# Kernel tuning notes

Measured on AMD Instinct MI355X. Metric: run time of the kernel, lower is better.

Reference implementation:

```python
import jax, jax.numpy as jnp
import numpy as np

N_NODES = 100000
N_EDGES = 1600000
IN_DIM = 7
HID = 64
OUT_DIM = 1
EPS = 1e-5  # BatchNorm1d eps


def setup_inputs() -> dict:
    key = jax.random.key(0)
    ks = jax.random.split(key, 16)
    x = jax.random.normal(ks[0], (N_NODES, IN_DIM), dtype=jnp.float32)
    edge_index = jax.random.randint(ks[1], (2, N_EDGES), 0, N_NODES)

    def lin(k, din, dout):
        # Glorot-ish init for a [din, dout] weight (x @ W convention)
        return jax.random.normal(k, (din, dout), dtype=jnp.float32) / np.float32(np.sqrt(din))

    inp = {"x": x, "edge_index": edge_index}
    dims = [(IN_DIM, HID), (HID, HID), (HID, HID)]
    i = 2
    for l, (din, dout) in enumerate(dims):
        inp[f"Wl{l}"] = lin(ks[i], din, dout); i += 1   # SAGEConv lin_l (applied to aggregated neighbors), carries bias
        inp[f"bl{l}"] = jnp.zeros((dout,), jnp.float32)
        inp[f"Wr{l}"] = lin(ks[i], din, dout); i += 1   # SAGEConv lin_r (root/self weight, no bias)
        inp[f"g{l}"] = jnp.ones((dout,), jnp.float32)   # BN gamma
        inp[f"be{l}"] = jnp.zeros((dout,), jnp.float32) # BN beta
    inp["Wo"] = lin(ks[i], HID, OUT_DIM); i += 1
    inp["bo"] = jnp.zeros((OUT_DIM,), jnp.float32)
    return inp


def _sage_bn_relu(x, src, dst, Wl, bl, Wr, g, be):
    # SAGEConv(aggr='mean'): out = lin_l(mean_{j->i} x_j) + lin_r(x_i)
    n = x.shape[0]
    msg = x[src]                                               # [E, d] gather
    s = jax.ops.segment_sum(msg, dst, num_segments=n)          # [N, d] scatter-add
    cnt = jax.ops.segment_sum(jnp.ones((src.shape[0],), x.dtype), dst, num_segments=n)
    agg = s / jnp.maximum(cnt, 1.0)[:, None]                   # scatter-mean (isolated nodes -> 0)
    h = agg @ Wl + bl + x @ Wr
    # BatchNorm1d (training-mode batch statistics over nodes)
    mu = h.mean(axis=0)
    var = h.var(axis=0)
    h = g * (h - mu) * jax.lax.rsqrt(var + EPS) + be
    return jax.nn.relu(h)


def reference(x, edge_index, Wl0, bl0, Wr0, g0, be0, Wl1, bl1, Wr1, g1, be1, Wl2, bl2, Wr2, g2, be2, Wo, bo):
    src, dst = edge_index[0], edge_index[1]
    h = _sage_bn_relu(x, src, dst, Wl0, bl0, Wr0, g0, be0)
    h = _sage_bn_relu(h, src, dst, Wl1, bl1, Wr1, g1, be1)
    h = _sage_bn_relu(h, src, dst, Wl2, bl2, Wr2, g2, be2)
    return h @ Wo + bo                                         # [N, 1]
```

## Files before the change

kernel.cpp:

```cpp
#include <hip/hip_runtime.h>

#define EPSV 1e-5f
#define REP 8
#define SBCAP 1280
#define CWIN 16640

static __device__ __forceinline__ ushort f2bf(float f) {
    unsigned u = __float_as_uint(f);
    unsigned r = (u + 0x7FFF + ((u >> 16) & 1)) >> 16;
    return (ushort)r;
}


__global__ __launch_bounds__(256) void sb_scatter(
    const int* __restrict__ src, const int* __restrict__ dst,
    int* __restrict__ sbcnt, int* __restrict__ bbuf, int E, int NSB)
{
    __shared__ int hist[512];
    __shared__ int gbase[512];
    int t = threadIdx.x;
    int r = blockIdx.x & (REP - 1);
    for (int i = t; i < NSB; i += 256) hist[i] = 0;
    __syncthreads();

    int base_i = (blockIdx.x * 256 + t) * 8;
    int d[8], s[8], rk[8];
    int m = E - base_i; m = m < 0 ? 0 : (m > 8 ? 8 : m);
    if (m == 8) {
        int4 da = *reinterpret_cast<const int4*>(dst + base_i);
        int4 db = *reinterpret_cast<const int4*>(dst + base_i + 4);
        int4 sa = *reinterpret_cast<const int4*>(src + base_i);
        int4 sb4 = *reinterpret_cast<const int4*>(src + base_i + 4);
        d[0] = da.x; d[1] = da.y; d[2] = da.z; d[3] = da.w;
        d[4] = db.x; d[5] = db.y; d[6] = db.z; d[7] = db.w;
        s[0] = sa.x; s[1] = sa.y; s[2] = sa.z; s[3] = sa.w;
        s[4] = sb4.x; s[5] = sb4.y; s[6] = sb4.z; s[7] = sb4.w;
    } else {
        for (int k = 0; k < m; ++k) { d[k] = dst[base_i + k]; s[k] = src[base_i + k]; }
    }
    for (int k = 0; k < m; ++k)
        rk[k] = atomicAdd(&hist[d[k] >> 9], 1);
    __syncthreads();

    for (int i = t; i < NSB; i += 256) {
        int c = hist[i];
        gbase[i] = c ? atomicAdd(&sbcnt[(r * NSB + i) * 16], c) : 0;
    }
    __syncthreads();

    for (int k = 0; k < m; ++k) {
        int sbk = d[k] >> 9;
        int pos = gbase[sbk] + rk[k];
        if (pos < SBCAP)
            bbuf[(size_t)(r * NSB + sbk) * SBCAP + pos] = ((d[k] & 511) << 17) | s[k];
    }
}

__global__ __launch_bounds__(512) void sb_build(
    const int* __restrict__ sbcnt, const int* __restrict__ bbuf,
    int2* __restrict__ seg, int* __restrict__ col, int n, int NSB)
{
    __shared__ int cnt[512], off[512], cur[512];
    int sb = blockIdx.x;
    int node0 = sb << 9;
    int t = threadIdx.x;
    cnt[t] = 0;
    __syncthreads();

    for (int r = 0; r < REP; ++r) {
        int c = min(sbcnt[(r * NSB + sb) * 16], SBCAP);
        const int* __restrict__ w = bbuf + (size_t)(r * NSB + sb) * SBCAP;
        for (int i = t; i < c; i += 512) atomicAdd(&cnt[w[i] >> 17], 1);
    }
    __syncthreads();

    if (t < 64) {
        int v[8]; int run = 0;
#pragma unroll
        for (int k = 0; k < 8; ++k) {
            v[k] = run;
            run += (cnt[t * 8 + k] + 15) & ~15;
        }
        int pre = run;
        for (int dd = 1; dd < 64; dd <<= 1) {
            int tm = __shfl_up(pre, dd);
            if (t >= dd) pre += tm;
        }
        int lane_excl = pre - run;
#pragma unroll
        for (int k = 0; k < 8; ++k) off[t * 8 + k] = lane_excl + v[k];
    }
    __syncthreads();

    int colbase = sb * CWIN;
    {
        int node = node0 + t;
        if (node < n) seg[node] = make_int2(colbase + off[t], cnt[t]);
        cur[t] = off[t];
    }
    __syncthreads();

    for (int r = 0; r < REP; ++r) {
        int c = min(sbcnt[(r * NSB + sb) * 16], SBCAP);
        const int* __restrict__ w = bbuf + (size_t)(r * NSB + sb) * SBCAP;
        for (int i = t; i < c; i += 512) {
            int e = w[i];
            int p = atomicAdd(&cur[e >> 17], 1);
            col[colbase + p] = e & 0x1FFFF;
        }
    }
    __syncthreads();
    {
        int pend = off[t] + ((cnt[t] + 15) & ~15);
        for (int p = off[t] + cnt[t]; p < pend; ++p) col[colbase + p] = n;
    }
}


__global__ __launch_bounds__(512) void transform7(
    const float* __restrict__ x,
    const float* __restrict__ Wl, const float* __restrict__ bl, const float* __restrict__ Wr,
    ushort* __restrict__ yl, float* __restrict__ h, int n)
{
    __shared__ float swl[7 * 64], swr[7 * 64], sbl[64];
    for (int i = threadIdx.x; i < 7 * 64; i += 512) { swl[i] = Wl[i]; swr[i] = Wr[i]; }
    if (threadIdx.x < 64) sbl[threadIdx.x] = bl[threadIdx.x];
    __syncthreads();

    if (blockIdx.x == 0 && threadIdx.x < 64) yl[(size_t)n * 64 + threadIdx.x] = 0;

    int lane = threadIdx.x & 63;
    int node = blockIdx.x * 8 + (threadIdx.x >> 6);
    if (node >= n) return;

    float xv = (lane < 7) ? x[(size_t)node * 7 + lane] : 0.f;
    float hl = 0.f, hr = sbl[lane];
#pragma unroll
    for (int k = 0; k < 7; ++k) {
        float xk = __shfl(xv, k);
        hl += xk * swl[k * 64 + lane];
        hr += xk * swr[k * 64 + lane];
    }
    yl[(size_t)node * 64 + lane] = f2bf(hl);
    h[(size_t)node * 64 + lane] = hr;
}


__global__ __launch_bounds__(256) void transform64(
    const float* __restrict__ zin, const float* __restrict__ scale, const float* __restrict__ shift,
    const float* __restrict__ Wl, const float* __restrict__ Wr, const float* __restrict__ bl,
    ushort* __restrict__ yl, float* __restrict__ h, int n)
{
    __shared__ float zt[64][68];
    __shared__ float swl[64 * 64];
    __shared__ float swr[64 * 64];
    __shared__ float ssc[64], ssh[64], sbl[64];

    int t = threadIdx.x;
    if (t < 64) { ssc[t] = scale[t]; ssh[t] = shift[t]; sbl[t] = bl[t]; }
    for (int i = t; i < 4096; i += 256) { swl[i] = Wl[i]; swr[i] = Wr[i]; }
    __syncthreads();

    int node0 = blockIdx.x * 64;
    {
        int m = t >> 2, c4 = (t & 3) * 16;
        int gm = node0 + m;
        if (gm < n) {
            const float4* zp = reinterpret_cast<const float4*>(zin + (size_t)gm * 64 + c4);
#pragma unroll
            for (int j = 0; j < 4; ++j) {
                float4 v = zp[j];
                int c = c4 + j * 4;
                v.x = fmaxf(v.x * ssc[c + 0] + ssh[c + 0], 0.f);
                v.y = fmaxf(v.y * ssc[c + 1] + ssh[c + 1], 0.f);
                v.z = fmaxf(v.z * ssc[c + 2] + ssh[c + 2], 0.f);
                v.w = fmaxf(v.w * ssc[c + 3] + ssh[c + 3], 0.f);
                zt[m][c + 0] = v.x; zt[m][c + 1] = v.y; zt[m][c + 2] = v.z; zt[m][c + 3] = v.w;
            }
        } else {
#pragma unroll
            for (int j = 0; j < 16; ++j) zt[m][c4 + j] = 0.f;
        }
    }
    __syncthreads();

    int ng = t >> 4;
    int cg = t & 15;
    int mb = ng * 4;
    const float* sw = (cg < 8) ? swl : swr;
    int c0 = (cg & 7) * 8;

    float acc[4][8];
#pragma unroll
    for (int i = 0; i < 4; ++i)
#pragma unroll
        for (int j = 0; j < 8; ++j) acc[i][j] = 0.f;

#pragma unroll 4
    for (int k = 0; k < 64; ++k) {
        float z0 = zt[mb + 0][k];
        float z1 = zt[mb + 1][k];
        float z2 = zt[mb + 2][k];
        float z3 = zt[mb + 3][k];
        float4 wa = *reinterpret_cast<const float4*>(sw + k * 64 + c0);
        float4 wb = *reinterpret_cast<const float4*>(sw + k * 64 + c0 + 4);
        float w[8] = {wa.x, wa.y, wa.z, wa.w, wb.x, wb.y, wb.z, wb.w};
#pragma unroll
        for (int j = 0; j < 8; ++j) {
            acc[0][j] += z0 * w[j];
            acc[1][j] += z1 * w[j];
            acc[2][j] += z2 * w[j];
            acc[3][j] += z3 * w[j];
        }
    }

#pragma unroll
    for (int i = 0; i < 4; ++i) {
        int gm = node0 + mb + i;
        if (gm >= n) continue;
        if (cg < 8) {
            uint4 pk;
            pk.x = (unsigned)f2bf(acc[i][0]) | ((unsigned)f2bf(acc[i][1]) << 16);
            pk.y = (unsigned)f2bf(acc[i][2]) | ((unsigned)f2bf(acc[i][3]) << 16);
            pk.z = (unsigned)f2bf(acc[i][4]) | ((unsigned)f2bf(acc[i][5]) << 16);
            pk.w = (unsigned)f2bf(acc[i][6]) | ((unsigned)f2bf(acc[i][7]) << 16);
            *reinterpret_cast<uint4*>(yl + (size_t)gm * 64 + c0) = pk;
        } else {
            float* dp = h + (size_t)gm * 64 + c0;
            *reinterpret_cast<float4*>(dp) =
                make_float4(acc[i][0] + sbl[c0 + 0], acc[i][1] + sbl[c0 + 1],
                            acc[i][2] + sbl[c0 + 2], acc[i][3] + sbl[c0 + 3]);
            *reinterpret_cast<float4*>(dp + 4) =
                make_float4(acc[i][4] + sbl[c0 + 4], acc[i][5] + sbl[c0 + 5],
                            acc[i][6] + sbl[c0 + 6], acc[i][7] + sbl[c0 + 7]);
        }
    }
}


__global__ __launch_bounds__(512) void gather_kernel(
    const ushort* __restrict__ yl, float* __restrict__ h,
    const int* __restrict__ col, const int2* __restrict__ seg, int n)
{
    int lane = threadIdx.x & 63;
    int node0 = blockIdx.x * 16 + (threadIdx.x >> 6) * 2;
    if (node0 >= n) return;
    int node1 = node0 + 1;

    int4 sp = *reinterpret_cast<const int4*>(&seg[node0]);
    int s0 = __builtin_amdgcn_readfirstlane(sp.x);
    int d0 = __builtin_amdgcn_readfirstlane(sp.y);
    int s1 = __builtin_amdgcn_readfirstlane(sp.z);
    int d1 = __builtin_amdgcn_readfirstlane(sp.w);
    if (node1 >= n) d1 = 0;
    int pc0 = (d0 + 15) & ~15;
    int pc1 = (d1 + 15) & ~15;
    int pcm = max(pc0, pc1);
    const int* __restrict__ cp0 = col + s0;
    const int* __restrict__ cp1 = col + s1;

    bool hi = lane >= 32;
    unsigned cl = (unsigned)(lane & 31);
    const unsigned* __restrict__ ylu = reinterpret_cast<const unsigned*>(yl);

    float alo0 = 0.f, ahi0 = 0.f, alo1 = 0.f, ahi1 = 0.f;
    for (int j0 = 0; j0 < pcm; j0 += 16) {
        if (j0 < pc0) {
            int4 ia = *reinterpret_cast<const int4*>(cp0 + j0);
            int4 ib = *reinterpret_cast<const int4*>(cp0 + j0 + 4);
            int4 ic = *reinterpret_cast<const int4*>(cp0 + j0 + 8);
            int4 id = *reinterpret_cast<const int4*>(cp0 + j0 + 12);
            unsigned p0 = (unsigned)(hi ? ia.y : ia.x);
            unsigned p1 = (unsigned)(hi ? ia.w : ia.z);
            unsigned p2 = (unsigned)(hi ? ib.y : ib.x);
            unsigned p3 = (unsigned)(hi ? ib.w : ib.z);
            unsigned p4 = (unsigned)(hi ? ic.y : ic.x);
            unsigned p5 = (unsigned)(hi ? ic.w : ic.z);
            unsigned p6 = (unsigned)(hi ? id.y : id.x);
            unsigned p7 = (unsigned)(hi ? id.w : id.z);
            unsigned u0 = ylu[(p0 << 5) + cl];
            unsigned u1 = ylu[(p1 << 5) + cl];
            unsigned u2 = ylu[(p2 << 5) + cl];
            unsigned u3 = ylu[(p3 << 5) + cl];
            unsigned u4 = ylu[(p4 << 5) + cl];
            unsigned u5 = ylu[(p5 << 5) + cl];
            unsigned u6 = ylu[(p6 << 5) + cl];
            unsigned u7 = ylu[(p7 << 5) + cl];
            alo0 += __uint_as_float(u0 << 16);      ahi0 += __uint_as_float(u0 & 0xFFFF0000u);
            alo0 += __uint_as_float(u1 << 16);      ahi0 += __uint_as_float(u1 & 0xFFFF0000u);
            alo0 += __uint_as_float(u2 << 16);      ahi0 += __uint_as_float(u2 & 0xFFFF0000u);
            alo0 += __uint_as_float(u3 << 16);      ahi0 += __uint_as_float(u3 & 0xFFFF0000u);
            alo0 += __uint_as_float(u4 << 16);      ahi0 += __uint_as_float(u4 & 0xFFFF0000u);
            alo0 += __uint_as_float(u5 << 16);      ahi0 += __uint_as_float(u5 & 0xFFFF0000u);
            alo0 += __uint_as_float(u6 << 16);      ahi0 += __uint_as_float(u6 & 0xFFFF0000u);
            alo0 += __uint_as_float(u7 << 16);      ahi0 += __uint_as_float(u7 & 0xFFFF0000u);
        }
        if (j0 < pc1) {
            int4 ia = *reinterpret_cast<const int4*>(cp1 + j0);
            int4 ib = *reinterpret_cast<const int4*>(cp1 + j0 + 4);
            int4 ic = *reinterpret_cast<const int4*>(cp1 + j0 + 8);
            int4 id = *reinterpret_cast<const int4*>(cp1 + j0 + 12);
            unsigned p0 = (unsigned)(hi ? ia.y : ia.x);
            unsigned p1 = (unsigned)(hi ? ia.w : ia.z);
            unsigned p2 = (unsigned)(hi ? ib.y : ib.x);
            unsigned p3 = (unsigned)(hi ? ib.w : ib.z);
            unsigned p4 = (unsigned)(hi ? ic.y : ic.x);
            unsigned p5 = (unsigned)(hi ? ic.w : ic.z);
            unsigned p6 = (unsigned)(hi ? id.y : id.x);
            unsigned p7 = (unsigned)(hi ? id.w : id.z);
            unsigned u0 = ylu[(p0 << 5) + cl];
            unsigned u1 = ylu[(p1 << 5) + cl];
            unsigned u2 = ylu[(p2 << 5) + cl];
            unsigned u3 = ylu[(p3 << 5) + cl];
            unsigned u4 = ylu[(p4 << 5) + cl];
            unsigned u5 = ylu[(p5 << 5) + cl];
            unsigned u6 = ylu[(p6 << 5) + cl];
            unsigned u7 = ylu[(p7 << 5) + cl];
            alo1 += __uint_as_float(u0 << 16);      ahi1 += __uint_as_float(u0 & 0xFFFF0000u);
            alo1 += __uint_as_float(u1 << 16);      ahi1 += __uint_as_float(u1 & 0xFFFF0000u);
            alo1 += __uint_as_float(u2 << 16);      ahi1 += __uint_as_float(u2 & 0xFFFF0000u);
            alo1 += __uint_as_float(u3 << 16);      ahi1 += __uint_as_float(u3 & 0xFFFF0000u);
            alo1 += __uint_as_float(u4 << 16);      ahi1 += __uint_as_float(u4 & 0xFFFF0000u);
            alo1 += __uint_as_float(u5 << 16);      ahi1 += __uint_as_float(u5 & 0xFFFF0000u);
            alo1 += __uint_as_float(u6 << 16);      ahi1 += __uint_as_float(u6 & 0xFFFF0000u);
            alo1 += __uint_as_float(u7 << 16);      ahi1 += __uint_as_float(u7 & 0xFFFF0000u);
        }
    }
    alo0 += __shfl_xor(alo0, 32);
    ahi0 += __shfl_xor(ahi0, 32);
    alo1 += __shfl_xor(alo1, 32);
    ahi1 += __shfl_xor(ahi1, 32);

    int mynode = hi ? node1 : node0;
    int mydeg  = hi ? d1 : d0;
    float a    = hi ? alo1 : alo0;
    float b    = hi ? ahi1 : ahi0;
    if (mynode < n) {
        float inv = 1.f / (float)max(mydeg, 1);
        float2* hp = reinterpret_cast<float2*>(h + (size_t)mynode * 64 + 2 * cl);
        float2 hv = *hp;
        hv.x += a * inv;
        hv.y += b * inv;
        *hp = hv;
    }
}


__global__ __launch_bounds__(256) void bn_stats(const float* __restrict__ h,
                                                float* __restrict__ sums, int n) {
    __shared__ float ls[128];
    if (threadIdx.x < 128) ls[threadIdx.x] = 0.f;
    __syncthreads();
    size_t total = (size_t)n * 64;
    size_t stride = (size_t)gridDim.x * 1024;
    float s0 = 0.f, s1 = 0.f, s2 = 0.f, s3 = 0.f;
    float q0 = 0.f, q1 = 0.f, q2 = 0.f, q3 = 0.f;
    for (size_t i = (size_t)blockIdx.x * 1024 + (size_t)threadIdx.x * 4; i < total; i += stride) {
        float4 v = *reinterpret_cast<const float4*>(h + i);
        s0 += v.x; q0 += v.x * v.x;
        s1 += v.y; q1 += v.y * v.y;
        s2 += v.z; q2 += v.z * v.z;
        s3 += v.w; q3 += v.w * v.w;
    }
    int c = (threadIdx.x * 4) & 63;
    atomicAdd(&ls[c + 0], s0); atomicAdd(&ls[c + 1], s1);
    atomicAdd(&ls[c + 2], s2); atomicAdd(&ls[c + 3], s3);
    atomicAdd(&ls[64 + c + 0], q0); atomicAdd(&ls[64 + c + 1], q1);
    atomicAdd(&ls[64 + c + 2], q2); atomicAdd(&ls[64 + c + 3], q3);
    __syncthreads();
    if (threadIdx.x < 128) atomicAdd(&sums[threadIdx.x], ls[threadIdx.x]);
}

__global__ void bn_finalize(const float* __restrict__ sums, const float* __restrict__ g,
                            const float* __restrict__ be, float* __restrict__ scale,
                            float* __restrict__ shift, int n) {
    int c = threadIdx.x;
    if (c < 64) {
        float inv_n = 1.f / (float)n;
        float mu = sums[c] * inv_n;
        float var = sums[64 + c] * inv_n - mu * mu;
        float sc = g[c] * rsqrtf(var + EPSV);
        scale[c] = sc;
        shift[c] = be[c] - mu * sc;
    }
}


__global__ __launch_bounds__(256) void out_kernel(const float* __restrict__ h,
                                                  const float* __restrict__ scale,
                                                  const float* __restrict__ shift,
                                                  const float* __restrict__ Wo,
                                                  const float* __restrict__ bo,
                                                  float* __restrict__ out, int n) {
    int lane = threadIdx.x & 63;
    int wave = threadIdx.x >> 6;
    int node = blockIdx.x * 4 + wave;
    if (node >= n) return;
    float v = h[(size_t)node * 64 + lane];
    v = fmaxf(v * scale[lane] + shift[lane], 0.f);
    float p = v * Wo[lane];
    for (int d = 32; d > 0; d >>= 1) p += __shfl_xor(p, d);
    if (lane == 0) out[node] = p + bo[0];
}


extern "C" void kernel_launch(void* const* d_in, const int* in_sizes, int n_in,
                              void* d_out, int out_size, void* d_ws, size_t ws_size,
                              hipStream_t stream) {
    const float* x   = (const float*)d_in[0];
    const int*   ei  = (const int*)d_in[1];
    const float* Wl0 = (const float*)d_in[2];
    const float* bl0 = (const float*)d_in[3];
    const float* Wr0 = (const float*)d_in[4];
    const float* g0  = (const float*)d_in[5];
    const float* be0 = (const float*)d_in[6];
    const float* Wl1 = (const float*)d_in[7];
    const float* bl1 = (const float*)d_in[8];
    const float* Wr1 = (const float*)d_in[9];
    const float* g1  = (const float*)d_in[10];
    const float* be1 = (const float*)d_in[11];
    const float* Wl2 = (const float*)d_in[12];
    const float* bl2 = (const float*)d_in[13];
    const float* Wr2 = (const float*)d_in[14];
    const float* g2  = (const float*)d_in[15];
    const float* be2 = (const float*)d_in[16];
    const float* Wo  = (const float*)d_in[17];
    const float* bo  = (const float*)d_in[18];

    const int N = in_sizes[0] / 7;
    const int E = in_sizes[1] / 2;
    const int NSB = (N + 511) / 512;
    const int* srcp = ei;
    const int* dstp = ei + E;

    char* ws = (char*)d_ws;
    size_t off = 0;
    auto walloc = [&](size_t bytes) -> void* {
        void* p = ws + off;
        off = (off + bytes + 255) & ~(size_t)255;
        return p;
    };
    int*    sbcnt  = (int*)walloc((size_t)REP * NSB * 16 * sizeof(int));
    int*    bbuf   = (int*)walloc((size_t)REP * NSB * SBCAP * sizeof(int));
    int2*   seg    = (int2*)walloc((size_t)(N + 1) * sizeof(int2));
    int*    col    = (int*)walloc((size_t)NSB * CWIN * sizeof(int));
    float*  sums   = (float*)walloc(3 * 128 * sizeof(float));
    float*  scale  = (float*)walloc(3 * 64 * sizeof(float));
    float*  shift  = (float*)walloc(3 * 64 * sizeof(float));
    ushort* yl     = (ushort*)walloc(((size_t)N + 1) * 64 * sizeof(ushort));
    float*  h0     = (float*)walloc((size_t)N * 64 * sizeof(float));
    float*  h1     = (float*)walloc((size_t)N * 64 * sizeof(float));

    hipMemsetAsync(sbcnt, 0, (size_t)REP * NSB * 16 * sizeof(int), stream);
    hipMemsetAsync(sums, 0, 3 * 128 * sizeof(float), stream);

    sb_scatter<<<(E + 2047) / 2048, 256, 0, stream>>>(srcp, dstp, sbcnt, bbuf, E, NSB);
    sb_build<<<NSB, 512, 0, stream>>>(sbcnt, bbuf, seg, col, N, NSB);

    const int gw  = (N + 7) / 8;
    const int gw2 = (N + 15) / 16;
    const int gt  = (N + 63) / 64;

    transform7<<<gw, 512, 0, stream>>>(x, Wl0, bl0, Wr0, yl, h0, N);
    gather_kernel<<<gw2, 512, 0, stream>>>(yl, h0, col, seg, N);
    bn_stats<<<1024, 256, 0, stream>>>(h0, sums, N);
    bn_finalize<<<1, 64, 0, stream>>>(sums, g0, be0, scale, shift, N);

    transform64<<<gt, 256, 0, stream>>>(h0, scale, shift, Wl1, Wr1, bl1, yl, h1, N);
    gather_kernel<<<gw2, 512, 0, stream>>>(yl, h1, col, seg, N);
    bn_stats<<<1024, 256, 0, stream>>>(h1, sums + 128, N);
    bn_finalize<<<1, 64, 0, stream>>>(sums + 128, g1, be1, scale + 64, shift + 64, N);

    transform64<<<gt, 256, 0, stream>>>(h1, scale + 64, shift + 64, Wl2, Wr2, bl2, yl, h0, N);
    gather_kernel<<<gw2, 512, 0, stream>>>(yl, h0, col, seg, N);
    bn_stats<<<1024, 256, 0, stream>>>(h0, sums + 256, N);
    bn_finalize<<<1, 64, 0, stream>>>(sums + 256, g2, be2, scale + 128, shift + 128, N);

    out_kernel<<<(N + 3) / 4, 256, 0, stream>>>(h0, scale + 128, shift + 128, Wo, bo, (float*)d_out, N);
}
```

Measured before the change: 357.6 us.

## Fuse BatchNorm statistics into gather kernel with persistent grid and 16B row loads

Folds the BN sum and sum-of-squares reduction into the neighbor-gather kernel, so the separate bn_stats pass that re-read the full hidden tensor is removed. The gather is also restructured: one wave per node in a grid-stride loop over a fixed 1024-block grid, with each lane loading a 16-byte chunk of a neighbor row (8 lanes per row, 8 neighbors in flight) and a shuffle reduction across neighbor groups. The cost is extra shuffle reductions per node, only 16 of 64 lanes active in the writeback, and a fixed grid that may underfill or load-imbalance.

Result: faster. 323.8 us (-9.4%).

```diff
diff --git a/kernel.cpp b/kernel.cpp
--- a/kernel.cpp
+++ b/kernel.cpp
@@ -240,135 +240,74 @@
 
 __global__ __launch_bounds__(512) void gather_kernel(
     const ushort* __restrict__ yl, float* __restrict__ h,
-    const int* __restrict__ col, const int2* __restrict__ seg, int n)
+    const int* __restrict__ col, const int2* __restrict__ seg,
+    float* __restrict__ sums, int n)
 {
-    int lane = threadIdx.x & 63;
-    int node0 = blockIdx.x * 16 + (threadIdx.x >> 6) * 2;
-    if (node0 >= n) return;
-    int node1 = node0 + 1;
-
-    int4 sp = *reinterpret_cast<const int4*>(&seg[node0]);
-    int s0 = __builtin_amdgcn_readfirstlane(sp.x);
-    int d0 = __builtin_amdgcn_readfirstlane(sp.y);
-    int s1 = __builtin_amdgcn_readfirstlane(sp.z);
-    int d1 = __builtin_amdgcn_readfirstlane(sp.w);
-    if (node1 >= n) d1 = 0;
-    int pc0 = (d0 + 15) & ~15;
-    int pc1 = (d1 + 15) & ~15;
-    int pcm = max(pc0, pc1);
-    const int* __restrict__ cp0 = col + s0;
-    const int* __restrict__ cp1 = col + s1;
-
-    bool hi = lane >= 32;
-    unsigned cl = (unsigned)(lane & 31);
+    __shared__ float ls[128];
+    int t = threadIdx.x;
+    if (t < 128) ls[t] = 0.f;
+    __syncthreads();
+
+    int lane = t & 63;
+    int g = lane >> 3, s = lane & 7;
     const unsigned* __restrict__ ylu = reinterpret_cast<const unsigned*>(yl);
 
-    float alo0 = 0.f, ahi0 = 0.f, alo1 = 0.f, ahi1 = 0.f;
-    for (int j0 = 0; j0 < pcm; j0 += 16) {
-        if (j0 < pc0) {
-            int4 ia = *reinterpret_cast<const int4*>(cp0 + j0);
-            int4 ib = *reinterpret_cast<const int4*>(cp0 + j0 + 4);
-            int4 ic = *reinterpret_cast<const int4*>(cp0 + j0 + 8);
-            int4 id = *reinterpret_cast<const int4*>(cp0 + j0 + 12);
-            unsigned p0 = (unsigned)(hi ? ia.y : ia.x);
-            unsigned p1 = (unsigned)(hi ? ia.w : ia.z);
-            unsigned p2 = (unsigned)(hi ? ib.y : ib.x);
-            unsigned p3 = (unsigned)(hi ? ib.w : ib.z);
-            unsigned p4 = (unsigned)(hi ? ic.y : ic.x);
-            unsigned p5 = (unsigned)(hi ? ic.w : ic.z);
-            unsigned p6 = (unsigned)(hi ? id.y : id.x);
-            unsigned p7 = (unsigned)(hi ? id.w : id.z);
-            unsigned u0 = ylu[(p0 << 5) + cl];
-            unsigned u1 = ylu[(p1 << 5) + cl];
-            unsigned u2 = ylu[(p2 << 5) + cl];
-            unsigned u3 = ylu[(p3 << 5) + cl];
-            unsigned u4 = ylu[(p4 << 5) + cl];
-            unsigned u5 = ylu[(p5 << 5) + cl];
-            unsigned u6 = ylu[(p6 << 5) + cl];
-            unsigned u7 = ylu[(p7 << 5) + cl];
-            alo0 += __uint_as_float(u0 << 16);      ahi0 += __uint_as_float(u0 & 0xFFFF0000u);
-            alo0 += __uint_as_float(u1 << 16);      ahi0 += __uint_as_float(u1 & 0xFFFF0000u);
-            alo0 += __uint_as_float(u2 << 16);      ahi0 += __uint_as_float(u2 & 0xFFFF0000u);
-            alo0 += __uint_as_float(u3 << 16);      ahi0 += __uint_as_float(u3 & 0xFFFF0000u);
-            alo0 += __uint_as_float(u4 << 16);      ahi0 += __uint_as_float(u4 & 0xFFFF0000u);
-            alo0 += __uint_as_float(u5 << 16);      ahi0 += __uint_as_float(u5 & 0xFFFF0000u);
-            alo0 += __uint_as_float(u6 << 16);      ahi0 += __uint_as_float(u6 & 0xFFFF0000u);
-            alo0 += __uint_as_float(u7 << 16);      ahi0 += __uint_as_float(u7 & 0xFFFF0000u);
-        }
-        if (j0 < pc1) {
-            int4 ia = *reinterpret_cast<const int4*>(cp1 + j0);
-            int4 ib = *reinterpret_cast<const int4*>(cp1 + j0 + 4);
-            int4 ic = *reinterpret_cast<const int4*>(cp1 + j0 + 8);
-            int4 id = *reinterpret_cast<const int4*>(cp1 + j0 + 12);
-            unsigned p0 = (unsigned)(hi ? ia.y : ia.x);
-            unsigned p1 = (unsigned)(hi ? ia.w : ia.z);
-            unsigned p2 = (unsigned)(hi ? ib.y : ib.x);
-            unsigned p3 = (unsigned)(hi ? ib.w : ib.z);
-            unsigned p4 = (unsigned)(hi ? ic.y : ic.x);
-            unsigned p5 = (unsigned)(hi ? ic.w : ic.z);
-            unsigned p6 = (unsigned)(hi ? id.y : id.x);
-            unsigned p7 = (unsigned)(hi ? id.w : id.z);
-            unsigned u0 = ylu[(p0 << 5) + cl];
-            unsigned u1 = ylu[(p1 << 5) + cl];
-            unsigned u2 = ylu[(p2 << 5) + cl];
-            unsigned u3 = ylu[(p3 << 5) + cl];
-            unsigned u4 = ylu[(p4 << 5) + cl];
-            unsigned u5 = ylu[(p5 << 5) + cl];
-            unsigned u6 = ylu[(p6 << 5) + cl];
-            unsigned u7 = ylu[(p7 << 5) + cl];
-            alo1 += __uint_as_float(u0 << 16);      ahi1 += __uint_as_float(u0 & 0xFFFF0000u);
-            alo1 += __uint_as_float(u1 << 16);      ahi1 += __uint_as_float(u1 & 0xFFFF0000u);
-            alo1 += __uint_as_float(u2 << 16);      ahi1 += __uint_as_float(u2 & 0xFFFF0000u);
-            alo1 += __uint_as_float(u3 << 16);      ahi1 += __uint_as_float(u3 & 0xFFFF0000u);
-            alo1 += __uint_as_float(u4 << 16);      ahi1 += __uint_as_float(u4 & 0xFFFF0000u);
-            alo1 += __uint_as_float(u5 << 16);      ahi1 += __uint_as_float(u5 & 0xFFFF0000u);
-            alo1 += __uint_as_float(u6 << 16);      ahi1 += __uint_as_float(u6 & 0xFFFF0000u);
-            alo1 += __uint_as_float(u7 << 16);      ahi1 += __uint_as_float(u7 & 0xFFFF0000u);
-        }
-    }
-    alo0 += __shfl_xor(alo0, 32);
-    ahi0 += __shfl_xor(ahi0, 32);
-    alo1 += __shfl_xor(alo1, 32);
-    ahi1 += __shfl_xor(ahi1, 32);
-
-    int mynode = hi ? node1 : node0;
-    int mydeg  = hi ? d1 : d0;
-    float a    = hi ? alo1 : alo0;
-    float b    = hi ? ahi1 : ahi0;
-    if (mynode < n) {
-        float inv = 1.f / (float)max(mydeg, 1);
-        float2* hp = reinterpret_cast<float2*>(h + (size_t)mynode * 64 + 2 * cl);
-        float2 hv = *hp;
-        hv.x += a * inv;
-        hv.y += b * inv;
-        *hp = hv;
-    }
-}
-
-
-__global__ __launch_bounds__(256) void bn_stats(const float* __restrict__ h,
-                                                float* __restrict__ sums, int n) {
-    __shared__ float ls[128];
-    if (threadIdx.x < 128) ls[threadIdx.x] = 0.f;
-    __syncthreads();
-    size_t total = (size_t)n * 64;
-    size_t stride = (size_t)gridDim.x * 1024;
-    float s0 = 0.f, s1 = 0.f, s2 = 0.f, s3 = 0.f;
-    float q0 = 0.f, q1 = 0.f, q2 = 0.f, q3 = 0.f;
-    for (size_t i = (size_t)blockIdx.x * 1024 + (size_t)threadIdx.x * 4; i < total; i += stride) {
-        float4 v = *reinterpret_cast<const float4*>(h + i);
-        s0 += v.x; q0 += v.x * v.x;
-        s1 += v.y; q1 += v.y * v.y;
-        s2 += v.z; q2 += v.z * v.z;
-        s3 += v.w; q3 += v.w * v.w;
-    }
-    int c = (threadIdx.x * 4) & 63;
-    atomicAdd(&ls[c + 0], s0); atomicAdd(&ls[c + 1], s1);
-    atomicAdd(&ls[c + 2], s2); atomicAdd(&ls[c + 3], s3);
-    atomicAdd(&ls[64 + c + 0], q0); atomicAdd(&ls[64 + c + 1], q1);
-    atomicAdd(&ls[64 + c + 2], q2); atomicAdd(&ls[64 + c + 3], q3);
-    __syncthreads();
-    if (threadIdx.x < 128) atomicAdd(&sums[threadIdx.x], ls[threadIdx.x]);
+    float ss0 = 0.f, ss1 = 0.f, ss2 = 0.f, ss3 = 0.f;
+    float sq0 = 0.f, sq1 = 0.f, sq2 = 0.f, sq3 = 0.f;
+
+    int nw = gridDim.x * 8;
+    for (int node = blockIdx.x * 8 + (t >> 6); node < n; node += nw) {
+        int2 sc = seg[node];
+        int s0  = __builtin_amdgcn_readfirstlane(sc.x);
+        int deg = __builtin_amdgcn_readfirstlane(sc.y);
+        int pc  = (deg + 15) & ~15;
+        const int* __restrict__ cp = col + s0;
+
+        float a0 = 0.f, a1 = 0.f, a2 = 0.f, a3 = 0.f;
+        float a4 = 0.f, a5 = 0.f, a6 = 0.f, a7 = 0.f;
+        for (int j0 = 0; j0 < pc; j0 += 16) {
+            int i0 = cp[j0 + g];
+            int i1 = cp[j0 + 8 + g];
+            uint4 ua = *reinterpret_cast<const uint4*>(ylu + ((size_t)i0 << 5) + s * 4);
+            uint4 ub = *reinterpret_cast<const uint4*>(ylu + ((size_t)i1 << 5) + s * 4);
+            a0 += __uint_as_float(ua.x << 16);        a1 += __uint_as_float(ua.x & 0xFFFF0000u);
+            a2 += __uint_as_float(ua.y << 16);        a3 += __uint_as_float(ua.y & 0xFFFF0000u);
+            a4 += __uint_as_float(ua.z << 16);        a5 += __uint_as_float(ua.z & 0xFFFF0000u);
+            a6 += __uint_as_float(ua.w << 16);        a7 += __uint_as_float(ua.w & 0xFFFF0000u);
+            a0 += __uint_as_float(ub.x << 16);        a1 += __uint_as_float(ub.x & 0xFFFF0000u);
+            a2 += __uint_as_float(ub.y << 16);        a3 += __uint_as_float(ub.y & 0xFFFF0000u);
+            a4 += __uint_as_float(ub.z << 16);        a5 += __uint_as_float(ub.z & 0xFFFF0000u);
+            a6 += __uint_as_float(ub.w << 16);        a7 += __uint_as_float(ub.w & 0xFFFF0000u);
+        }
+#pragma unroll
+        for (int mk = 8; mk <= 32; mk <<= 1) {
+            a0 += __shfl_xor(a0, mk); a1 += __shfl_xor(a1, mk);
+            a2 += __shfl_xor(a2, mk); a3 += __shfl_xor(a3, mk);
+            a4 += __shfl_xor(a4, mk); a5 += __shfl_xor(a5, mk);
+            a6 += __shfl_xor(a6, mk); a7 += __shfl_xor(a7, mk);
+        }
+        if (g < 2) {
+            float inv = 1.f / (float)max(deg, 1);
+            float b0 = (g ? a4 : a0), b1 = (g ? a5 : a1), b2 = (g ? a6 : a2), b3 = (g ? a7 : a3);
+            float* hp = h + (size_t)node * 64 + s * 8 + g * 4;
+            float4 hv = *reinterpret_cast<float4*>(hp);
+            hv.x += b0 * inv; hv.y += b1 * inv; hv.z += b2 * inv; hv.w += b3 * inv;
+            *reinterpret_cast<float4*>(hp) = hv;
+            ss0 += hv.x; sq0 += hv.x * hv.x;
+            ss1 += hv.y; sq1 += hv.y * hv.y;
+            ss2 += hv.z; sq2 += hv.z * hv.z;
+            ss3 += hv.w; sq3 += hv.w * hv.w;
+        }
+    }
+    if (g < 2) {
+        int cb = s * 8 + g * 4;
+        atomicAdd(&ls[cb + 0], ss0); atomicAdd(&ls[cb + 1], ss1);
+        atomicAdd(&ls[cb + 2], ss2); atomicAdd(&ls[cb + 3], ss3);
+        atomicAdd(&ls[64 + cb + 0], sq0); atomicAdd(&ls[64 + cb + 1], sq1);
+        atomicAdd(&ls[64 + cb + 2], sq2); atomicAdd(&ls[64 + cb + 3], sq3);
+    }
+    __syncthreads();
+    if (t < 128) atomicAdd(&sums[t], ls[t]);
 }
 
 __global__ void bn_finalize(const float* __restrict__ sums, const float* __restrict__ g,
@@ -458,22 +397,19 @@
     sb_build<<<NSB, 512, 0, stream>>>(sbcnt, bbuf, seg, col, N, NSB);
 
     const int gw  = (N + 7) / 8;
-    const int gw2 = (N + 15) / 16;
+    const int gp  = 1024;
     const int gt  = (N + 63) / 64;
 
     transform7<<<gw, 512, 0, stream>>>(x, Wl0, bl0, Wr0, yl, h0, N);
-    gather_kernel<<<gw2, 512, 0, stream>>>(yl, h0, col, seg, N);
-    bn_stats<<<1024, 256, 0, stream>>>(h0, sums, N);
+    gather_kernel<<<gp, 512, 0, stream>>>(yl, h0, col, seg, sums, N);
     bn_finalize<<<1, 64, 0, stream>>>(sums, g0, be0, scale, shift, N);
 
     transform64<<<gt, 256, 0, stream>>>(h0, scale, shift, Wl1, Wr1, bl1, yl, h1, N);
-    gather_kernel<<<gw2, 512, 0, stream>>>(yl, h1, col, seg, N);
-    bn_stats<<<1024, 256, 0, stream>>>(h1, sums + 128, N);
+    gather_kernel<<<gp, 512, 0, stream>>>(yl, h1, col, seg, sums + 128, N);
     bn_finalize<<<1, 64, 0, stream>>>(sums + 128, g1, be1, scale + 64, shift + 64, N);
 
     transform64<<<gt, 256, 0, stream>>>(h1, scale + 64, shift + 64, Wl2, Wr2, bl2, yl, h0, N);
-    gather_kernel<<<gw2, 512, 0, stream>>>(yl, h0, col, seg, N);
-    bn_stats<<<1024, 256, 0, stream>>>(h0, sums + 256, N);
+    gather_kernel<<<gp, 512, 0, stream>>>(yl, h0, col, seg, sums + 256, N);
     bn_finalize<<<1, 64, 0, stream>>>(sums + 256, g2, be2, scale + 128, shift + 128, N);
 
     out_kernel<<<(N + 3) / 4, 256, 0, stream>>>(h0, scale + 128, shift + 128, Wo, bo, (float*)d_out, N);
```
